# Kernel tuning notes

Measured on AMD Instinct MI355X. Metric: run time of the kernel, lower is better.

## Reference

```python
import jax, jax.numpy as jnp
import numpy as np

HEAD_DIM = 32
SCALE = HEAD_DIM ** -0.5


def setup_inputs() -> dict:
    key = jax.random.key(0)
    x = jax.random.normal(key, (4, 2048, 1536), dtype=jnp.float32)
    return {"x": x}


def reference(x):
    B, N, C3 = x.shape
    C = C3 // 3
    H = C // HEAD_DIM
    # [B, N, 3, H, hd] -> [3, B, H, N, hd]
    qkv = x.reshape(B, N, 3, H, HEAD_DIM).transpose(2, 0, 3, 1, 4)
    q, k, v = qkv[0], qkv[1], qkv[2]
    attn = jnp.einsum("bhnd,bhmd->bhnm", q, k) * SCALE  # [B,H,N,N]
    attn = jax.nn.softmax(attn, axis=-1)
    out = jnp.einsum("bhnm,bhmd->bhnd", attn, v)  # [B,H,N,hd]
    return out.transpose(0, 2, 1, 3).reshape(B, N, C)
```

## Files before the change

kernel.cpp:

```cpp
#include <hip/hip_runtime.h>

namespace {

constexpr int Bb   = 4;
constexpr int Nn   = 2048;
constexpr int Hh   = 16;
constexpr int Dd   = 32;
constexpr int C3   = 1536;
constexpr int Cc   = 512;
constexpr int QBLK = 64;
constexpr int KBLK = 32;
constexpr int NIT  = Nn / KBLK;
constexpr float THR = 8.0f;

using f16 = _Float16;
typedef f16   f16x2 __attribute__((ext_vector_type(2)));
typedef f16   f16x4 __attribute__((ext_vector_type(4)));
typedef f16   f16x8 __attribute__((ext_vector_type(8)));
typedef float f32x4 __attribute__((ext_vector_type(4)));

#if __has_builtin(__builtin_amdgcn_exp2f)
__device__ __forceinline__ float fexp2(float x) { return __builtin_amdgcn_exp2f(x); }
#else
__device__ __forceinline__ float fexp2(float x) { return exp2f(x); }
#endif

__device__ __forceinline__ f16x4 pk4(float a, float b, float c, float d) {
  f16x2 lo = __builtin_bit_cast(f16x2, __builtin_amdgcn_cvt_pkrtz(a, b));
  f16x2 hi = __builtin_bit_cast(f16x2, __builtin_amdgcn_cvt_pkrtz(c, d));
  f16x4 r;
  r[0] = lo[0]; r[1] = lo[1]; r[2] = hi[0]; r[3] = hi[1];
  return r;
}

#define MFMA16(a, b, c) __builtin_amdgcn_mfma_f32_16x16x16f16((a), (b), (c), 0, 0, 0)
#define MFMA32(a, b, c) __builtin_amdgcn_mfma_f32_16x16x32_f16((a), (b), (c), 0, 0, 0)

constexpr int KST = 80;
constexpr int VST = 72;

__global__ __launch_bounds__(256, 8) void attn_fwd(const float* __restrict__ x,
                                                   float* __restrict__ out) {
  __shared__ unsigned char ldsK[2][KBLK * KST];
  __shared__ unsigned char ldsV[2][Dd * VST];

  const int tid  = threadIdx.x;
  const int lane = tid & 63;
  const int wv   = tid >> 6;
  const int m    = lane & 15;
  const int g    = lane >> 4;

  const int bx = blockIdx.x;
  const int bh = bx & 63;
  const int qb = bx >> 6;
  const int b  = bh >> 4;
  const int h  = bh & 15;

  const float* xb = x + (size_t)b * Nn * C3;
  const float* kp = xb + Cc + h * Dd;
  const float* vp = xb + 2 * Cc + h * Dd;

  const float qs = 0.17677669529663687f * 1.4426950408889634f;
  const int qrow = qb * QBLK + wv * 16 + m;
  const float* qr = xb + (size_t)qrow * C3 + h * Dd + g * 8;
  float4 qa = *(const float4*)qr;
  float4 qc = *(const float4*)(qr + 4);
  f16x8 qf;
  {
    f16x4 lo = pk4(qa.x * qs, qa.y * qs, qa.z * qs, qa.w * qs);
    f16x4 hi = pk4(qc.x * qs, qc.y * qs, qc.z * qs, qc.w * qs);
    qf[0] = lo[0]; qf[1] = lo[1]; qf[2] = lo[2]; qf[3] = lo[3];
    qf[4] = hi[0]; qf[5] = hi[1]; qf[6] = hi[2]; qf[7] = hi[3];
  }

  const int skey = tid >> 3;
  const int sd4  = (tid & 7) * 4;
  const float* kgp = kp + (size_t)skey * C3 + sd4;
  const float* vgp = vp + (size_t)skey * C3 + sd4;

  const f16x4 ones = {(f16)1.f, (f16)1.f, (f16)1.f, (f16)1.f};

  f32x4 acc0 = {};
  f32x4 acc1 = {};
  f32x4 lsum = {};
  float mrun = 0.f;

  {
    float4 kf = *(const float4*)kgp;
    float4 vf = *(const float4*)vgp;
    *(f16x4*)(ldsK[0] + skey * KST + sd4 * 2) = pk4(kf.x, kf.y, kf.z, kf.w);
    unsigned char* vw = ldsV[0] + sd4 * VST + skey * 2;
    *(f16*)(vw + 0 * VST) = (f16)vf.x;
    *(f16*)(vw + 1 * VST) = (f16)vf.y;
    *(f16*)(vw + 2 * VST) = (f16)vf.z;
    *(f16*)(vw + 3 * VST) = (f16)vf.w;
  }
  __syncthreads();

  int cur = 0;
#pragma unroll 2
  for (int it = 0; it < NIT; ++it) {
    if (it + 1 < NIT) { kgp += KBLK * C3; vgp += KBLK * C3; }
    float4 kf = *(const float4*)kgp;
    float4 vf = *(const float4*)vgp;

    const unsigned char* Kb = ldsK[cur];
    const unsigned char* Vb = ldsV[cur];

    f16x8 ka0 = *(const f16x8*)(Kb + m * KST + g * 16);
    f16x8 ka1 = *(const f16x8*)(Kb + (16 + m) * KST + g * 16);
    f16x4 va00 = *(const f16x4*)(Vb + m * VST + (4 * g) * 2);
    f16x4 va01 = *(const f16x4*)(Vb + m * VST + (16 + 4 * g) * 2);
    f16x4 va10 = *(const f16x4*)(Vb + (16 + m) * VST + (4 * g) * 2);
    f16x4 va11 = *(const f16x4*)(Vb + (16 + m) * VST + (16 + 4 * g) * 2);

    f32x4 cvec = {-mrun, -mrun, -mrun, -mrun};
    f32x4 s0 = MFMA32(ka0, qf, cvec);
    f32x4 s1 = MFMA32(ka1, qf, cvec);

    float tl = fmaxf(fmaxf(fmaxf(s0[0], s0[1]), fmaxf(s0[2], s0[3])),
                     fmaxf(fmaxf(s1[0], s1[1]), fmaxf(s1[2], s1[3])));
    if (__builtin_expect(__any(tl > THR), 0)) {
      float t = fmaxf(tl, __shfl_xor(tl, 16));
      t = fmaxf(t, __shfl_xor(t, 32));
      float d = fmaxf(t, 0.f);
      float al = fexp2(-d);
#pragma unroll
      for (int r = 0; r < 4; ++r) {
        acc0[r] *= al; acc1[r] *= al; lsum[r] *= al;
        s0[r] -= d; s1[r] -= d;
      }
      mrun += d;
    }

    f32x4 p0, p1;
#pragma unroll
    for (int r = 0; r < 4; ++r) p0[r] = fexp2(s0[r]);
#pragma unroll
    for (int r = 0; r < 4; ++r) p1[r] = fexp2(s1[r]);

    f16x4 pb0 = pk4(p0[0], p0[1], p0[2], p0[3]);
    f16x4 pb1 = pk4(p1[0], p1[1], p1[2], p1[3]);

    acc0 = MFMA16(va00, pb0, acc0);
    acc0 = MFMA16(va01, pb1, acc0);
    acc1 = MFMA16(va10, pb0, acc1);
    acc1 = MFMA16(va11, pb1, acc1);
    lsum = MFMA16(ones, pb0, lsum);
    lsum = MFMA16(ones, pb1, lsum);

    *(f16x4*)(ldsK[cur ^ 1] + skey * KST + sd4 * 2) = pk4(kf.x, kf.y, kf.z, kf.w);
    unsigned char* vw = ldsV[cur ^ 1] + sd4 * VST + skey * 2;
    *(f16*)(vw + 0 * VST) = (f16)vf.x;
    *(f16*)(vw + 1 * VST) = (f16)vf.y;
    *(f16*)(vw + 2 * VST) = (f16)vf.z;
    *(f16*)(vw + 3 * VST) = (f16)vf.w;
    __syncthreads();
    cur ^= 1;
  }

  float inv = 1.0f / lsum[0];
  float* op = out + ((size_t)b * Nn + qrow) * Cc + h * Dd;
  f32x4 o0, o1;
#pragma unroll
  for (int r = 0; r < 4; ++r) { o0[r] = acc0[r] * inv; o1[r] = acc1[r] * inv; }
  *(f32x4*)(op + g * 4)      = o0;
  *(f32x4*)(op + 16 + g * 4) = o1;
}

}

extern "C" void kernel_launch(void* const* d_in, const int* in_sizes, int n_in,
                              void* d_out, int out_size, void* d_ws, size_t ws_size,
                              hipStream_t stream) {
  const float* x = (const float*)d_in[0];
  float* outp    = (float*)d_out;
  attn_fwd<<<dim3(Bb * Hh * (Nn / QBLK)), dim3(256), 0, stream>>>(x, outp);
}
```

Measured before the change: 152.1 us.

## Process two query tiles per wave to reuse K/V LDS loads

Doubles the query block to 128 rows so each wave handles two 16-row query tiles that share the same K and V fragments read from LDS. This halves the global K/V traffic and LDS staging per query row. The V staging is re-indexed so each thread loads strided scalar elements and writes them to LDS with a stride of 8 rows. The rescale threshold is raised, and occupancy drops because launch bounds go to 4 and there are fewer blocks (1024) with more registers each.

```diff
diff --git a/kernel.cpp b/kernel.cpp
--- a/kernel.cpp
+++ b/kernel.cpp
@@ -8,10 +8,10 @@
 constexpr int Dd   = 32;
 constexpr int C3   = 1536;
 constexpr int Cc   = 512;
-constexpr int QBLK = 64;
+constexpr int QBLK = 128;
 constexpr int KBLK = 32;
 constexpr int NIT  = Nn / KBLK;
-constexpr float THR = 8.0f;
+constexpr float THR = 11.0f;
 
 using f16 = _Float16;
 typedef f16   f16x2 __attribute__((ext_vector_type(2)));
@@ -39,7 +39,7 @@
 constexpr int KST = 80;
 constexpr int VST = 72;
 
-__global__ __launch_bounds__(256, 8) void attn_fwd(const float* __restrict__ x,
+__global__ __launch_bounds__(256, 4) void attn_fwd(const float* __restrict__ x,
                                                    float* __restrict__ out) {
   __shared__ unsigned char ldsK[2][KBLK * KST];
   __shared__ unsigned char ldsV[2][Dd * VST];
@@ -57,115 +57,125 @@
   const int h  = bh & 15;
 
   const float* xb = x + (size_t)b * Nn * C3;
-  const float* kp = xb + Cc + h * Dd;
-  const float* vp = xb + 2 * Cc + h * Dd;
+  const float* xk = xb + Cc + h * Dd;
+  const float* xv = xb + 2 * Cc + h * Dd;
 
   const float qs = 0.17677669529663687f * 1.4426950408889634f;
-  const int qrow = qb * QBLK + wv * 16 + m;
-  const float* qr = xb + (size_t)qrow * C3 + h * Dd + g * 8;
-  float4 qa = *(const float4*)qr;
-  float4 qc = *(const float4*)(qr + 4);
-  f16x8 qf;
-  {
+  const int qrow0 = qb * QBLK + wv * 32;
+  f16x8 qf[2];
+#pragma unroll
+  for (int mt = 0; mt < 2; ++mt) {
+    const float* qr = xb + (size_t)(qrow0 + mt * 16 + m) * C3 + h * Dd + g * 8;
+    float4 qa = *(const float4*)qr;
+    float4 qc = *(const float4*)(qr + 4);
     f16x4 lo = pk4(qa.x * qs, qa.y * qs, qa.z * qs, qa.w * qs);
     f16x4 hi = pk4(qc.x * qs, qc.y * qs, qc.z * qs, qc.w * qs);
-    qf[0] = lo[0]; qf[1] = lo[1]; qf[2] = lo[2]; qf[3] = lo[3];
-    qf[4] = hi[0]; qf[5] = hi[1]; qf[6] = hi[2]; qf[7] = hi[3];
+    qf[mt][0] = lo[0]; qf[mt][1] = lo[1]; qf[mt][2] = lo[2]; qf[mt][3] = lo[3];
+    qf[mt][4] = hi[0]; qf[mt][5] = hi[1]; qf[mt][6] = hi[2]; qf[mt][7] = hi[3];
   }
 
   const int skey = tid >> 3;
   const int sd4  = (tid & 7) * 4;
-  const float* kgp = kp + (size_t)skey * C3 + sd4;
-  const float* vgp = vp + (size_t)skey * C3 + sd4;
+  const int sdv  = tid & 7;
+  const int kofs = skey * C3 + sd4;
+  const int vofs = skey * C3 + sdv;
 
   const f16x4 ones = {(f16)1.f, (f16)1.f, (f16)1.f, (f16)1.f};
 
-  f32x4 acc0 = {};
-  f32x4 acc1 = {};
-  f32x4 lsum = {};
-  float mrun = 0.f;
+  f32x4 acc[2][2] = {};
+  f32x4 lsum[2] = {};
+  f32x4 negm[2] = {};
 
   {
-    float4 kf = *(const float4*)kgp;
-    float4 vf = *(const float4*)vgp;
+    float4 kf = *(const float4*)(xk + kofs);
+    float v0 = xv[vofs], v1 = xv[vofs + 8], v2 = xv[vofs + 16], v3 = xv[vofs + 24];
     *(f16x4*)(ldsK[0] + skey * KST + sd4 * 2) = pk4(kf.x, kf.y, kf.z, kf.w);
-    unsigned char* vw = ldsV[0] + sd4 * VST + skey * 2;
-    *(f16*)(vw + 0 * VST) = (f16)vf.x;
-    *(f16*)(vw + 1 * VST) = (f16)vf.y;
-    *(f16*)(vw + 2 * VST) = (f16)vf.z;
-    *(f16*)(vw + 3 * VST) = (f16)vf.w;
+    unsigned char* vw = ldsV[0] + sdv * VST + skey * 2;
+    *(f16*)(vw + 0 * 8 * VST) = (f16)v0;
+    *(f16*)(vw + 1 * 8 * VST) = (f16)v1;
+    *(f16*)(vw + 2 * 8 * VST) = (f16)v2;
+    *(f16*)(vw + 3 * 8 * VST) = (f16)v3;
   }
   __syncthreads();
 
   int cur = 0;
 #pragma unroll 2
   for (int it = 0; it < NIT; ++it) {
-    if (it + 1 < NIT) { kgp += KBLK * C3; vgp += KBLK * C3; }
-    float4 kf = *(const float4*)kgp;
-    float4 vf = *(const float4*)vgp;
+    const int nx = (it + 1 < NIT) ? it + 1 : it;
+    const float* xk2 = xk + nx * KBLK * C3;
+    const float* xv2 = xv + nx * KBLK * C3;
+    float4 kf = *(const float4*)(xk2 + kofs);
+    float v0 = xv2[vofs], v1 = xv2[vofs + 8], v2 = xv2[vofs + 16], v3 = xv2[vofs + 24];
 
     const unsigned char* Kb = ldsK[cur];
     const unsigned char* Vb = ldsV[cur];
 
     f16x8 ka0 = *(const f16x8*)(Kb + m * KST + g * 16);
     f16x8 ka1 = *(const f16x8*)(Kb + (16 + m) * KST + g * 16);
-    f16x4 va00 = *(const f16x4*)(Vb + m * VST + (4 * g) * 2);
-    f16x4 va01 = *(const f16x4*)(Vb + m * VST + (16 + 4 * g) * 2);
-    f16x4 va10 = *(const f16x4*)(Vb + (16 + m) * VST + (4 * g) * 2);
-    f16x4 va11 = *(const f16x4*)(Vb + (16 + m) * VST + (16 + 4 * g) * 2);
+    f16x4 va00 = *(const f16x4*)(Vb + m * VST + 8 * g);
+    f16x4 va01 = *(const f16x4*)(Vb + m * VST + 32 + 8 * g);
+    f16x4 va10 = *(const f16x4*)(Vb + (16 + m) * VST + 8 * g);
+    f16x4 va11 = *(const f16x4*)(Vb + (16 + m) * VST + 32 + 8 * g);
 
-    f32x4 cvec = {-mrun, -mrun, -mrun, -mrun};
-    f32x4 s0 = MFMA32(ka0, qf, cvec);
-    f32x4 s1 = MFMA32(ka1, qf, cvec);
+#pragma unroll
+    for (int mt = 0; mt < 2; ++mt) {
+      f32x4 s0 = MFMA32(ka0, qf[mt], negm[mt]);
+      f32x4 s1 = MFMA32(ka1, qf[mt], negm[mt]);
 
-    float tl = fmaxf(fmaxf(fmaxf(s0[0], s0[1]), fmaxf(s0[2], s0[3])),
-                     fmaxf(fmaxf(s1[0], s1[1]), fmaxf(s1[2], s1[3])));
-    if (__builtin_expect(__any(tl > THR), 0)) {
-      float t = fmaxf(tl, __shfl_xor(tl, 16));
-      t = fmaxf(t, __shfl_xor(t, 32));
-      float d = fmaxf(t, 0.f);
-      float al = fexp2(-d);
+      float a1 = fmaxf(fmaxf(s0[0], s0[1]), s0[2]);
+      float a2 = fmaxf(fmaxf(s0[3], s1[0]), s1[1]);
+      float a3 = fmaxf(fmaxf(s1[2], s1[3]), a1);
+      float tl = fmaxf(a2, a3);
+      if (__builtin_expect(__any(tl > THR), 0)) {
+        float t = fmaxf(tl, __shfl_xor(tl, 16));
+        t = fmaxf(t, __shfl_xor(t, 32));
+        float d = fmaxf(t, 0.f);
+        float al = fexp2(-d);
 #pragma unroll
-      for (int r = 0; r < 4; ++r) {
-        acc0[r] *= al; acc1[r] *= al; lsum[r] *= al;
-        s0[r] -= d; s1[r] -= d;
+        for (int r = 0; r < 4; ++r) {
+          acc[mt][0][r] *= al; acc[mt][1][r] *= al; lsum[mt][r] *= al;
+          s0[r] -= d; s1[r] -= d;
+          negm[mt][r] -= d;
+        }
       }
-      mrun += d;
+
+      f32x4 p0, p1;
+#pragma unroll
+      for (int r = 0; r < 4; ++r) p0[r] = fexp2(s0[r]);
+#pragma unroll
+      for (int r = 0; r < 4; ++r) p1[r] = fexp2(s1[r]);
+
+      f16x4 pb0 = pk4(p0[0], p0[1], p0[2], p0[3]);
+      f16x4 pb1 = pk4(p1[0], p1[1], p1[2], p1[3]);
+
+      acc[mt][0] = MFMA16(va00, pb0, acc[mt][0]);
+      acc[mt][0] = MFMA16(va01, pb1, acc[mt][0]);
+      acc[mt][1] = MFMA16(va10, pb0, acc[mt][1]);
+      acc[mt][1] = MFMA16(va11, pb1, acc[mt][1]);
+      lsum[mt] = MFMA16(ones, pb0, lsum[mt]);
+      lsum[mt] = MFMA16(ones, pb1, lsum[mt]);
     }
 
-    f32x4 p0, p1;
-#pragma unroll
-    for (int r = 0; r < 4; ++r) p0[r] = fexp2(s0[r]);
-#pragma unroll
-    for (int r = 0; r < 4; ++r) p1[r] = fexp2(s1[r]);
-
-    f16x4 pb0 = pk4(p0[0], p0[1], p0[2], p0[3]);
-    f16x4 pb1 = pk4(p1[0], p1[1], p1[2], p1[3]);
-
-    acc0 = MFMA16(va00, pb0, acc0);
-    acc0 = MFMA16(va01, pb1, acc0);
-    acc1 = MFMA16(va10, pb0, acc1);
-    acc1 = MFMA16(va11, pb1, acc1);
-    lsum = MFMA16(ones, pb0, lsum);
-    lsum = MFMA16(ones, pb1, lsum);
-
     *(f16x4*)(ldsK[cur ^ 1] + skey * KST + sd4 * 2) = pk4(kf.x, kf.y, kf.z, kf.w);
-    unsigned char* vw = ldsV[cur ^ 1] + sd4 * VST + skey * 2;
-    *(f16*)(vw + 0 * VST) = (f16)vf.x;
-    *(f16*)(vw + 1 * VST) = (f16)vf.y;
-    *(f16*)(vw + 2 * VST) = (f16)vf.z;
-    *(f16*)(vw + 3 * VST) = (f16)vf.w;
+    unsigned char* vw = ldsV[cur ^ 1] + sdv * VST + skey * 2;
+    *(f16*)(vw + 0 * 8 * VST) = (f16)v0;
+    *(f16*)(vw + 1 * 8 * VST) = (f16)v1;
+    *(f16*)(vw + 2 * 8 * VST) = (f16)v2;
+    *(f16*)(vw + 3 * 8 * VST) = (f16)v3;
     __syncthreads();
     cur ^= 1;
   }
 
-  float inv = 1.0f / lsum[0];
-  float* op = out + ((size_t)b * Nn + qrow) * Cc + h * Dd;
-  f32x4 o0, o1;
 #pragma unroll
-  for (int r = 0; r < 4; ++r) { o0[r] = acc0[r] * inv; o1[r] = acc1[r] * inv; }
-  *(f32x4*)(op + g * 4)      = o0;
-  *(f32x4*)(op + 16 + g * 4) = o1;
+  for (int mt = 0; mt < 2; ++mt) {
+    float inv = 1.0f / lsum[mt][0];
+    float* op = out + ((size_t)b * Nn + (qrow0 + mt * 16 + m)) * Cc + h * Dd;
+    f32x4 o0, o1;
+#pragma unroll
+    for (int r = 0; r < 4; ++r) { o0[r] = acc[mt][0][r] * inv; o1[r] = acc[mt][1][r] * inv; }
+    *(f32x4*)(op + g * 4)      = o0;
+    *(f32x4*)(op + 16 + g * 4) = o1;
+  }
 }
 
 }
```

New measurement: 138.5 us. -8.9%, faster.
